# Kernel optimization log

Hardware: AMD Instinct MI355X
Metric: run time of the kernel (lower is better)

Reference implementation:

```python
import jax, jax.numpy as jnp
import numpy as np

B, T, E, H = 16, 512, 4096, 8
HD = E // H  # 512; repo requires T <= HD due to mask buffer shape


def setup_inputs() -> dict:
    key = jax.random.key(0)
    ks = jax.random.split(key, 6)
    s_in = 1.0 / np.sqrt(E)
    data = jax.random.normal(ks[0], (B, T, E), dtype=jnp.float32)
    # per-head projection weights stacked: [H, E, HD], no bias (matches nn.Linear(bias=False))
    Wq = jax.random.normal(ks[1], (H, E, HD), dtype=jnp.float32) * s_in
    Wk = jax.random.normal(ks[2], (H, E, HD), dtype=jnp.float32) * s_in
    Wv = jax.random.normal(ks[3], (H, E, HD), dtype=jnp.float32) * s_in
    # output projection Linear(E, E): stored as [in, out] for y @ Wo + bo
    Wo = jax.random.normal(ks[4], (E, E), dtype=jnp.float32) * s_in
    bo = jax.random.normal(ks[5], (E,), dtype=jnp.float32) * 0.01
    return {"data": data, "Wq": Wq, "Wk": Wk, "Wv": Wv, "Wo": Wo, "bo": bo}


def reference(data, Wq, Wk, Wv, Wo, bo):
    # per-head projections: [B,H,T,HD]
    q = jnp.einsum('bte,hed->bhtd', data, Wq)
    k = jnp.einsum('bte,hed->bhtd', data, Wk)
    v = jnp.einsum('bte,hed->bhtd', data, Wv)
    # NOTE: repo scales by sqrt(EMBEDDING_SIZE), not sqrt(head_size)
    scores = jnp.einsum('bhtd,bhsd->bhts', q, k) / jnp.float32(np.sqrt(E))
    causal = jnp.tril(jnp.ones((T, T), dtype=bool))
    scores = jnp.where(causal, scores, jnp.float32(-jnp.inf))
    attn = jax.nn.softmax(scores, axis=-1)  # dropout is identity (p=0 / eval)
    out = jnp.einsum('bhts,bhsd->bhtd', attn, v)
    # concat heads along feature dim: [B,T,H*HD] == [B,T,E]
    out = out.transpose(0, 2, 1, 3).reshape(B, T, E)
    return out @ Wo + bo
```

## Files before the change

kernel.cpp:

```cpp
#include <hip/hip_runtime.h>
#include <stdint.h>

typedef __bf16  bf16x8 __attribute__((ext_vector_type(8)));
typedef unsigned short u16x8 __attribute__((ext_vector_type(8)));
typedef float   f32x4  __attribute__((ext_vector_type(4)));

__device__ __forceinline__ unsigned short f2b(float f) {
  union { float f; uint32_t u; } v; v.f = f;
  uint32_t r = v.u + 0x7fffu + ((v.u >> 16) & 1u);
  return (unsigned short)(r >> 16);
}
__device__ __forceinline__ float b2f(unsigned short u) {
  union { uint32_t u; float f; } v; v.u = ((uint32_t)u) << 16;
  return v.f;
}

#define GLDS16(gp, lp) __builtin_amdgcn_global_load_lds( \
    (const __attribute__((address_space(1))) void*)(gp), \
    (__attribute__((address_space(3))) void*)(lp), 16, 0, 0)

template <class Epi>
__device__ __forceinline__ void gemm_core(
    const unsigned short* __restrict__ A, int lda,
    const unsigned short* __restrict__ Bt, int ldb,
    int K, int r0, int c0, Epi epi)
{
  extern __shared__ unsigned short lds[];
  unsigned short* As = lds;
  unsigned short* Bs = lds + 128 * 64;
  const int tid  = threadIdx.x;
  const int lane = tid & 63;
  const int wave = tid >> 6;
  const int wr   = (wave >> 1) * 64;
  const int wc   = (wave & 1) * 64;
  const int quad = lane >> 4;
  const int lm   = lane & 15;

  int srow[4], scol[4], sbase[4];
#pragma unroll
  for (int s = 0; s < 4; s++) {
    int chunk = (wave * 4 + s) * 64 + lane;
    srow[s]  = chunk >> 3;
    scol[s]  = ((chunk & 7) ^ (srow[s] & 7)) * 8;
    sbase[s] = (wave * 4 + s) * 512;
  }

  f32x4 acc[4][4];
#pragma unroll
  for (int i = 0; i < 4; i++)
#pragma unroll
    for (int j = 0; j < 4; j++)
      acc[i][j] = (f32x4){0.f, 0.f, 0.f, 0.f};

  for (int k0 = 0; k0 < K; k0 += 64) {
    __syncthreads();
#pragma unroll
    for (int s = 0; s < 4; s++) {
      GLDS16(A  + (size_t)(r0 + srow[s]) * lda + k0 + scol[s], As + sbase[s]);
      GLDS16(Bt + (size_t)(c0 + srow[s]) * ldb + k0 + scol[s], Bs + sbase[s]);
    }
    __syncthreads();
#pragma unroll
    for (int kk = 0; kk < 64; kk += 32) {
      bf16x8 a[4], b[4];
      const int p = (((kk >> 3) + quad) ^ (lm & 7)) * 8;
#pragma unroll
      for (int i = 0; i < 4; i++)
        a[i] = *(const bf16x8*)&As[(wr + i * 16 + lm) * 64 + p];
#pragma unroll
      for (int j = 0; j < 4; j++)
        b[j] = *(const bf16x8*)&Bs[(wc + j * 16 + lm) * 64 + p];
#pragma unroll
      for (int i = 0; i < 4; i++)
#pragma unroll
        for (int j = 0; j < 4; j++)
          acc[i][j] = __builtin_amdgcn_mfma_f32_16x16x32_bf16(a[i], b[j], acc[i][j], 0, 0, 0);
    }
  }
#pragma unroll
  for (int i = 0; i < 4; i++)
#pragma unroll
    for (int j = 0; j < 4; j++)
#pragma unroll
      for (int r = 0; r < 4; r++)
        epi(r0 + wr + i * 16 + quad * 4 + r, c0 + wc + j * 16 + lm, acc[i][j][r]);
}

__global__ __launch_bounds__(256) void cvt_bf16_kernel(const float* __restrict__ in,
                                                       unsigned short* __restrict__ out) {
  size_t i = ((size_t)blockIdx.x * 256 + threadIdx.x) * 8;
  f32x4 a = *(const f32x4*)&in[i];
  f32x4 b = *(const f32x4*)&in[i + 4];
  u16x8 r;
  r[0] = f2b(a[0]); r[1] = f2b(a[1]); r[2] = f2b(a[2]); r[3] = f2b(a[3]);
  r[4] = f2b(b[0]); r[5] = f2b(b[1]); r[6] = f2b(b[2]); r[7] = f2b(b[3]);
  *(u16x8*)&out[i] = r;
}

__global__ __launch_bounds__(256) void tconv_kernel(const float* __restrict__ in,
                                                    unsigned short* __restrict__ out,
                                                    int R, int C) {
  __shared__ unsigned short tile[32][33];
  int r0 = blockIdx.y * 32, c0 = blockIdx.x * 32;
  const float* inz = in + (size_t)blockIdx.z * R * C;
  unsigned short* outz = out + (size_t)blockIdx.z * R * C;
  int tr = threadIdx.x >> 5;
  int tc = threadIdx.x & 31;
#pragma unroll
  for (int s = 0; s < 4; s++) {
    int r = tr + s * 8;
    tile[r][tc] = f2b(inz[(size_t)(r0 + r) * C + c0 + tc]);
  }
  __syncthreads();
#pragma unroll
  for (int s = 0; s < 4; s++) {
    int r = tr + s * 8;
    outz[(size_t)(c0 + r) * R + r0 + tc] = tile[tc][r];
  }
}

__global__ __launch_bounds__(256) void proj_kernel(const unsigned short* __restrict__ data,
                                                   const unsigned short* __restrict__ Wt,
                                                   unsigned short* __restrict__ q,
                                                   unsigned short* __restrict__ k,
                                                   unsigned short* __restrict__ vt) {
  int z = blockIdx.y;
  int p = z >> 3, h = z & 7;
  int r0 = blockIdx.z * 128, c0 = blockIdx.x * 128;
  const unsigned short* Bt = Wt + (size_t)z * 512 * 4096;
  if (p == 0) {
    unsigned short* dst = q + (size_t)h * 8192 * 512;
    gemm_core(data, 4096, Bt, 4096, 4096, r0, c0,
              [=](int row, int col, float v) { dst[(size_t)row * 512 + col] = f2b(v); });
  } else if (p == 1) {
    unsigned short* dst = k + (size_t)h * 8192 * 512;
    gemm_core(data, 4096, Bt, 4096, 4096, r0, c0,
              [=](int row, int col, float v) { dst[(size_t)row * 512 + col] = f2b(v); });
  } else {
    gemm_core(data, 4096, Bt, 4096, 4096, r0, c0,
              [=](int row, int col, float v) {
                vt[(((size_t)(h * 16 + (row >> 9)) * 512 + col) << 9) + (row & 511)] = f2b(v);
              });
  }
}

__global__ __launch_bounds__(256) void score_kernel(const unsigned short* __restrict__ q,
                                                    const unsigned short* __restrict__ k,
                                                    unsigned short* __restrict__ S) {
  int z = blockIdx.z;
  int h = z >> 4, b = z & 15;
  int r0 = blockIdx.y * 128, c0 = blockIdx.x * 128;
  if (c0 > r0 + 127) return;
  const unsigned short* A  = q + ((size_t)h * 8192 + b * 512) * 512;
  const unsigned short* Bt = k + ((size_t)h * 8192 + b * 512) * 512;
  unsigned short* Sz = S + (size_t)z * 262144;
  gemm_core(A, 512, Bt, 512, 512, r0, c0,
            [=](int row, int col, float v) { Sz[(size_t)row * 512 + col] = f2b(v * 0.015625f); });
}

__global__ __launch_bounds__(256) void softmax_kernel(unsigned short* __restrict__ S) {
  int row  = blockIdx.x * 4 + (threadIdx.x >> 6);
  int lane = threadIdx.x & 63;
  int t = row & 511;
  unsigned short* pr = S + (size_t)row * 512;
  u16x8 u = *(const u16x8*)&pr[lane * 8];
  float s[8];
  float m = -1e30f;
#pragma unroll
  for (int jj = 0; jj < 8; jj++) {
    int j = lane * 8 + jj;
    s[jj] = (j <= t) ? b2f(u[jj]) : -1e30f;
    m = fmaxf(m, s[jj]);
  }
#pragma unroll
  for (int o = 32; o > 0; o >>= 1) m = fmaxf(m, __shfl_xor(m, o, 64));
  float l = 0.f;
#pragma unroll
  for (int jj = 0; jj < 8; jj++) {
    int j = lane * 8 + jj;
    s[jj] = (j <= t) ? __expf(s[jj] - m) : 0.f;
    l += s[jj];
  }
#pragma unroll
  for (int o = 32; o > 0; o >>= 1) l += __shfl_xor(l, o, 64);
  float inv = 1.f / l;
  u16x8 r;
#pragma unroll
  for (int jj = 0; jj < 8; jj++) r[jj] = f2b(s[jj] * inv);
  *(u16x8*)&pr[lane * 8] = r;
}

__global__ __launch_bounds__(256) void av_kernel(const unsigned short* __restrict__ S,
                                                 const unsigned short* __restrict__ vt,
                                                 unsigned short* __restrict__ ao) {
  int z = blockIdx.z;
  int h = z >> 4, b = z & 15;
  int r0 = blockIdx.y * 128, c0 = blockIdx.x * 128;
  const unsigned short* A  = S + (size_t)z * 262144;
  const unsigned short* Bt = vt + (size_t)z * 262144;
  int K = r0 + 128;
  gemm_core(A, 512, Bt, 512, K, r0, c0,
            [=](int row, int col, float v) {
              ao[((size_t)(b * 512 + row)) * 4096 + h * 512 + col] = f2b(v);
            });
}

__global__ __launch_bounds__(256) void out_kernel(const unsigned short* __restrict__ ao,
                                                  const unsigned short* __restrict__ Wot,
                                                  const float* __restrict__ bo,
                                                  float* __restrict__ out) {
  int r0 = blockIdx.y * 128, c0 = blockIdx.x * 128;
  gemm_core(ao, 4096, Wot, 4096, 4096, r0, c0,
            [=](int row, int col, float v) { out[(size_t)row * 4096 + col] = v + bo[col]; });
}

extern "C" void kernel_launch(void* const* d_in, const int* in_sizes, int n_in,
                              void* d_out, int out_size, void* d_ws, size_t ws_size,
                              hipStream_t stream) {
  const float* data = (const float*)d_in[0];
  const float* Wq = (const float*)d_in[1];
  const float* Wk = (const float*)d_in[2];
  const float* Wv = (const float*)d_in[3];
  const float* Wo = (const float*)d_in[4];
  const float* bo = (const float*)d_in[5];
  float* out = (float*)d_out;

  char* w = (char*)d_ws;
  unsigned short* datab = (unsigned short*)(w);
  unsigned short* Wt    = (unsigned short*)(w + 67108864ULL);
  unsigned short* Wot   = (unsigned short*)(w + 167772160ULL);
  unsigned short* qb    = (unsigned short*)(w + 201326592ULL);
  unsigned short* kb    = (unsigned short*)(w + 268435456ULL);
  unsigned short* vtb   = (unsigned short*)(w + 335544320ULL);
  unsigned short* Sb    = Wt;
  unsigned short* aob   = datab;

  const size_t LDS_BYTES = 2 * 128 * 64 * sizeof(unsigned short);

  cvt_bf16_kernel<<<16384, 256, 0, stream>>>(data, datab);
  tconv_kernel<<<dim3(16, 128, 8), 256, 0, stream>>>(Wq, Wt, 4096, 512);
  tconv_kernel<<<dim3(16, 128, 8), 256, 0, stream>>>(Wk, Wt + (size_t)8 * 2097152, 4096, 512);
  tconv_kernel<<<dim3(16, 128, 8), 256, 0, stream>>>(Wv, Wt + (size_t)16 * 2097152, 4096, 512);
  tconv_kernel<<<dim3(128, 128, 1), 256, 0, stream>>>(Wo, Wot, 4096, 4096);

  proj_kernel<<<dim3(4, 24, 64), 256, LDS_BYTES, stream>>>(datab, Wt, qb, kb, vtb);
  score_kernel<<<dim3(4, 4, 128), 256, LDS_BYTES, stream>>>(qb, kb, Sb);
  softmax_kernel<<<16384, 256, 0, stream>>>(Sb);
  av_kernel<<<dim3(4, 4, 128), 256, LDS_BYTES, stream>>>(Sb, vtb, aob);
  out_kernel<<<dim3(32, 64, 1), 256, LDS_BYTES, stream>>>(aob, Wot, bo, out);
}
```

Baseline: 1.665 ms.

## Use 256x256-tile, 8-wave pipelined GEMM for projection and output kernels

Adds a new GEMM core with 256x256 output tiles, 512 threads and a double-buffered 128KB LDS staging area. Global-to-LDS loads are interleaved with MFMA phases and sequenced by explicit waitcnt, barriers and setprio. The projection and output kernels switch to this core. The goal is more data reuse per tile and better overlap of memory traffic with matrix math, at the cost of high register pressure, only one block per CU, and fewer blocks in the grid.

```diff
diff --git a/kernel.cpp b/kernel.cpp
--- a/kernel.cpp
+++ b/kernel.cpp
@@ -18,6 +18,140 @@
 #define GLDS16(gp, lp) __builtin_amdgcn_global_load_lds( \
     (const __attribute__((address_space(1))) void*)(gp), \
     (__attribute__((address_space(3))) void*)(lp), 16, 0, 0)
+
+template <class Epi>
+__device__ __forceinline__ void gemm256(
+    unsigned short* lds,
+    const unsigned short* __restrict__ A, int lda,
+    const unsigned short* __restrict__ Bt, int ldb,
+    int K, int r0, int c0, Epi epi)
+{
+  const int tid  = threadIdx.x;
+  const int lane = tid & 63;
+  const int wave = tid >> 6;
+  const int wm   = wave >> 2;
+  const int wn   = wave & 3;
+  const int quad = lane >> 4;
+  const int lm   = lane & 15;
+  const int sw   = (quad ^ ((lm >> 1) & 3)) * 8;
+  const int NT   = K >> 6;
+
+  size_t gA[2], gB[2];
+  int ldso[2];
+#pragma unroll
+  for (int s = 0; s < 2; s++) {
+    int ci = wave * 128 + s * 64 + lane;
+    int r  = ci >> 2;
+    int c  = (ci & 3) ^ ((r >> 1) & 3);
+    gA[s]   = (size_t)(r0 + r) * lda + c * 8;
+    gB[s]   = (size_t)(c0 + r) * ldb + c * 8;
+    ldso[s] = (wave * 2 + s) * 512;
+  }
+
+#define STG_A(t, kh) do { if ((t) < NT) {                         \
+    int _b = ((t) & 1) * 32768 + (kh) * 8192;                     \
+    size_t _ko = (size_t)(t) * 64 + (kh) * 32;                    \
+    GLDS16(A + gA[0] + _ko, lds + _b + ldso[0]);                  \
+    GLDS16(A + gA[1] + _ko, lds + _b + ldso[1]); } } while (0)
+#define STG_B(t, kh) do { if ((t) < NT) {                         \
+    int _b = ((t) & 1) * 32768 + 16384 + (kh) * 8192;             \
+    size_t _ko = (size_t)(t) * 64 + (kh) * 32;                    \
+    GLDS16(Bt + gB[0] + _ko, lds + _b + ldso[0]);                 \
+    GLDS16(Bt + gB[1] + _ko, lds + _b + ldso[1]); } } while (0)
+
+  f32x4 acc[8][4];
+#pragma unroll
+  for (int i = 0; i < 8; i++)
+#pragma unroll
+    for (int j = 0; j < 4; j++)
+      acc[i][j] = (f32x4){0.f, 0.f, 0.f, 0.f};
+
+  STG_A(0, 0); STG_B(0, 0); STG_A(0, 1); STG_B(0, 1);
+  STG_A(1, 0); STG_B(1, 0); STG_A(1, 1);
+  asm volatile("s_waitcnt vmcnt(6)" ::: "memory");
+  __builtin_amdgcn_s_barrier();
+
+  const int arow = (wm * 128 + lm) * 32 + sw;
+  const int brow = (wn * 64 + lm) * 32 + sw;
+
+  for (int t = 0; t < NT; ++t) {
+    const int Ab = (t & 1) * 32768;
+    const int Bb = Ab + 16384;
+    bf16x8 a[8], b[2];
+
+#pragma unroll
+    for (int i = 0; i < 8; i++) a[i] = *(const bf16x8*)&lds[Ab + arow + i * 512];
+    b[0] = *(const bf16x8*)&lds[Bb + brow];
+    b[1] = *(const bf16x8*)&lds[Bb + brow + 512];
+    STG_B(t + 1, 1);
+    __builtin_amdgcn_s_barrier();
+    asm volatile("s_waitcnt lgkmcnt(0)" ::: "memory");
+    __builtin_amdgcn_s_setprio(1);
+#pragma unroll
+    for (int i = 0; i < 8; i++) {
+      acc[i][0] = __builtin_amdgcn_mfma_f32_16x16x32_bf16(a[i], b[0], acc[i][0], 0, 0, 0);
+      acc[i][1] = __builtin_amdgcn_mfma_f32_16x16x32_bf16(a[i], b[1], acc[i][1], 0, 0, 0);
+    }
+    __builtin_amdgcn_s_setprio(0);
+    __builtin_amdgcn_s_barrier();
+
+    b[0] = *(const bf16x8*)&lds[Bb + brow + 1024];
+    b[1] = *(const bf16x8*)&lds[Bb + brow + 1536];
+    STG_A(t + 2, 0);
+    __builtin_amdgcn_s_barrier();
+    asm volatile("s_waitcnt lgkmcnt(0)" ::: "memory");
+    __builtin_amdgcn_s_setprio(1);
+#pragma unroll
+    for (int i = 0; i < 8; i++) {
+      acc[i][2] = __builtin_amdgcn_mfma_f32_16x16x32_bf16(a[i], b[0], acc[i][2], 0, 0, 0);
+      acc[i][3] = __builtin_amdgcn_mfma_f32_16x16x32_bf16(a[i], b[1], acc[i][3], 0, 0, 0);
+    }
+    __builtin_amdgcn_s_setprio(0);
+    __builtin_amdgcn_s_barrier();
+
+#pragma unroll
+    for (int i = 0; i < 8; i++) a[i] = *(const bf16x8*)&lds[Ab + 8192 + arow + i * 512];
+    b[0] = *(const bf16x8*)&lds[Bb + 8192 + brow];
+    b[1] = *(const bf16x8*)&lds[Bb + 8192 + brow + 512];
+    STG_B(t + 2, 0);
+    __builtin_amdgcn_s_barrier();
+    asm volatile("s_waitcnt lgkmcnt(0)" ::: "memory");
+    __builtin_amdgcn_s_setprio(1);
+#pragma unroll
+    for (int i = 0; i < 8; i++) {
+      acc[i][0] = __builtin_amdgcn_mfma_f32_16x16x32_bf16(a[i], b[0], acc[i][0], 0, 0, 0);
+      acc[i][1] = __builtin_amdgcn_mfma_f32_16x16x32_bf16(a[i], b[1], acc[i][1], 0, 0, 0);
+    }
+    __builtin_amdgcn_s_setprio(0);
+    __builtin_amdgcn_s_barrier();
+
+    b[0] = *(const bf16x8*)&lds[Bb + 8192 + brow + 1024];
+    b[1] = *(const bf16x8*)&lds[Bb + 8192 + brow + 1536];
+    STG_A(t + 2, 1);
+    if (t == NT - 2)     asm volatile("s_waitcnt vmcnt(0)" ::: "memory");
+    else if (t < NT - 2) asm volatile("s_waitcnt vmcnt(6)" ::: "memory");
+    __builtin_amdgcn_s_barrier();
+    asm volatile("s_waitcnt lgkmcnt(0)" ::: "memory");
+    __builtin_amdgcn_s_setprio(1);
+#pragma unroll
+    for (int i = 0; i < 8; i++) {
+      acc[i][2] = __builtin_amdgcn_mfma_f32_16x16x32_bf16(a[i], b[0], acc[i][2], 0, 0, 0);
+      acc[i][3] = __builtin_amdgcn_mfma_f32_16x16x32_bf16(a[i], b[1], acc[i][3], 0, 0, 0);
+    }
+    __builtin_amdgcn_s_setprio(0);
+    __builtin_amdgcn_s_barrier();
+  }
+
+#pragma unroll
+  for (int i = 0; i < 8; i++)
+#pragma unroll
+    for (int j = 0; j < 4; j++)
+#pragma unroll
+      for (int r = 0; r < 4; r++)
+        epi(r0 + wm * 128 + i * 16 + quad * 4 + r, c0 + wn * 64 + j * 16 + lm, acc[i][j][r]);
+#undef STG_A
+#undef STG_B
+}
 
 template <class Epi>
 __device__ __forceinline__ void gemm_core(
@@ -25,9 +159,9 @@
     const unsigned short* __restrict__ Bt, int ldb,
     int K, int r0, int c0, Epi epi)
 {
-  extern __shared__ unsigned short lds[];
-  unsigned short* As = lds;
-  unsigned short* Bs = lds + 128 * 64;
+  extern __shared__ unsigned short sds[];
+  unsigned short* As = sds;
+  unsigned short* Bs = sds + 128 * 64;
   const int tid  = threadIdx.x;
   const int lane = tid & 63;
   const int wave = tid >> 6;
@@ -119,28 +253,29 @@
   }
 }
 
-__global__ __launch_bounds__(256) void proj_kernel(const unsigned short* __restrict__ data,
+__global__ __launch_bounds__(512) void proj_kernel(const unsigned short* __restrict__ data,
                                                    const unsigned short* __restrict__ Wt,
                                                    unsigned short* __restrict__ q,
                                                    unsigned short* __restrict__ k,
                                                    unsigned short* __restrict__ vt) {
+  __shared__ unsigned short lds[65536];
   int z = blockIdx.y;
   int p = z >> 3, h = z & 7;
-  int r0 = blockIdx.z * 128, c0 = blockIdx.x * 128;
+  int r0 = blockIdx.z * 256, c0 = blockIdx.x * 256;
   const unsigned short* Bt = Wt + (size_t)z * 512 * 4096;
   if (p == 0) {
     unsigned short* dst = q + (size_t)h * 8192 * 512;
-    gemm_core(data, 4096, Bt, 4096, 4096, r0, c0,
-              [=](int row, int col, float v) { dst[(size_t)row * 512 + col] = f2b(v); });
+    gemm256(lds, data, 4096, Bt, 4096, 4096, r0, c0,
+            [=](int row, int col, float v) { dst[(size_t)row * 512 + col] = f2b(v); });
   } else if (p == 1) {
     unsigned short* dst = k + (size_t)h * 8192 * 512;
-    gemm_core(data, 4096, Bt, 4096, 4096, r0, c0,
-              [=](int row, int col, float v) { dst[(size_t)row * 512 + col] = f2b(v); });
+    gemm256(lds, data, 4096, Bt, 4096, 4096, r0, c0,
+            [=](int row, int col, float v) { dst[(size_t)row * 512 + col] = f2b(v); });
   } else {
-    gemm_core(data, 4096, Bt, 4096, 4096, r0, c0,
-              [=](int row, int col, float v) {
-                vt[(((size_t)(h * 16 + (row >> 9)) * 512 + col) << 9) + (row & 511)] = f2b(v);
-              });
+    gemm256(lds, data, 4096, Bt, 4096, 4096, r0, c0,
+            [=](int row, int col, float v) {
+              vt[(((size_t)(h * 16 + (row >> 9)) * 512 + col) << 9) + (row & 511)] = f2b(v);
+            });
   }
 }
 
@@ -205,13 +340,14 @@
             });
 }
 
-__global__ __launch_bounds__(256) void out_kernel(const unsigned short* __restrict__ ao,
+__global__ __launch_bounds__(512) void out_kernel(const unsigned short* __restrict__ ao,
                                                   const unsigned short* __restrict__ Wot,
                                                   const float* __restrict__ bo,
                                                   float* __restrict__ out) {
-  int r0 = blockIdx.y * 128, c0 = blockIdx.x * 128;
-  gemm_core(ao, 4096, Wot, 4096, 4096, r0, c0,
-            [=](int row, int col, float v) { out[(size_t)row * 4096 + col] = v + bo[col]; });
+  __shared__ unsigned short lds[65536];
+  int r0 = blockIdx.y * 256, c0 = blockIdx.x * 256;
+  gemm256(lds, ao, 4096, Wot, 4096, 4096, r0, c0,
+          [=](int row, int col, float v) { out[(size_t)row * 4096 + col] = v + bo[col]; });
 }
 
 extern "C" void kernel_launch(void* const* d_in, const int* in_sizes, int n_in,
@@ -243,9 +379,9 @@
   tconv_kernel<<<dim3(16, 128, 8), 256, 0, stream>>>(Wv, Wt + (size_t)16 * 2097152, 4096, 512);
   tconv_kernel<<<dim3(128, 128, 1), 256, 0, stream>>>(Wo, Wot, 4096, 4096);
 
-  proj_kernel<<<dim3(4, 24, 64), 256, LDS_BYTES, stream>>>(datab, Wt, qb, kb, vtb);
+  proj_kernel<<<dim3(2, 24, 32), 512, 0, stream>>>(datab, Wt, qb, kb, vtb);
   score_kernel<<<dim3(4, 4, 128), 256, LDS_BYTES, stream>>>(qb, kb, Sb);
   softmax_kernel<<<16384, 256, 0, stream>>>(Sb);
   av_kernel<<<dim3(4, 4, 128), 256, LDS_BYTES, stream>>>(Sb, vtb, aob);
-  out_kernel<<<dim3(32, 64, 1), 256, LDS_BYTES, stream>>>(aob, Wot, bo, out);
-}
+  out_kernel<<<dim3(16, 32, 1), 512, 0, stream>>>(aob, Wot, bo, out);
+}
```

Result: faster. 1.468 ms (-11.8%).
